# Performance work log

Measured on AMD Instinct MI355X. Metric: run time of the kernel, lower is better.

The kernel has to match this reference:

```python
import jax, jax.numpy as jnp
import numpy as np
from math import sqrt

RELATIVE_CUTOFF = 128
VALUE_DIM = 64


def _skew(m):
    # m: (b, h, S, 2S-1) -> (b, h, S, S), out[i, j] = m[i, j - i + S - 1]
    b, h, S, _ = m.shape
    m = jnp.pad(m, ((0, 0), (0, 0), (0, 0), (0, 1)))          # (b,h,S,2S)
    m = m.reshape(b, h, 2 * S * S)
    m = jnp.pad(m, ((0, 0), (0, 0), (0, S - 1)))
    m = m.reshape(b, h, S + 1, 2 * S - 1)
    return m[:, :, :S, S - 1:]


def setup_inputs() -> dict:
    key = jax.random.key(0)
    ks = jax.random.split(key, 5)
    B, S, E, H, Dk, Dv = 2, 2048, 512, 8, 64, 64
    return {
        "xs": jax.random.normal(ks[0], (B, S, E), dtype=jnp.float32),
        "w_q": jax.random.normal(ks[1], (H, E, Dk), dtype=jnp.float32) * (1.0 / sqrt(E)),
        "w_k": jax.random.normal(ks[2], (H, E, Dk), dtype=jnp.float32) * (1.0 / sqrt(E)),
        "w_v": jax.random.normal(ks[3], (H, E, Dv), dtype=jnp.float32) * (1.0 / sqrt(E)),
        "w_o": jnp.ones((H,), dtype=jnp.float32),
        "a_k": jax.random.normal(ks[4], (2 * RELATIVE_CUTOFF + 1, Dk), dtype=jnp.float32) * 0.1,
    }


def reference(xs, w_q, w_k, w_v, w_o, a_k):
    S = xs.shape[1]
    queries = jnp.einsum("bse,heq->bhsq", xs, w_q)
    keys = jnp.einsum("bse,hek->bhsk", xs, w_k)
    values = jnp.einsum("bse,hev->bhsv", xs, w_v)

    # relative positional embeddings: pos in [-S+1, S-1], clamped to cutoff
    pos = jnp.clip(jnp.arange(-S + 1, S), -RELATIVE_CUTOFF, RELATIVE_CUTOFF) + RELATIVE_CUTOFF
    rel = a_k[pos]                                             # (2S-1, Dk)

    q_k = jnp.einsum("bhiq,bhjq->bhij", queries, keys)
    q_rel = _skew(jnp.einsum("bhiq,rq->bhir", queries, rel))   # (b,h,S,S)

    e = (q_k + q_rel) / sqrt(VALUE_DIM)
    alphas = jax.nn.softmax(e, axis=3)
    z = jnp.einsum("bhij,bhjv->bhiv", alphas, values)
    return jnp.einsum("bhsv,h->bsv", z, w_o)
```

## Files before the change

kernel.cpp:

```cpp
#include <hip/hip_runtime.h>
#include <hip/hip_bf16.h>

#define S_LEN 2048
#define E_DIM 512
#define D_DIM 64
#define H_NUM 8
#define B_NUM 2
#define BH_NUM 16
#define NQA 257
#define QAE_W 512
#define KSPLIT 2
#define KV_PER (S_LEN / KSPLIT)
#define NT (KV_PER / 64)
#define QTILE 256

typedef _Float16 half8 __attribute__((ext_vector_type(8)));
typedef float f32x16 __attribute__((ext_vector_type(16)));
typedef unsigned int uint2v __attribute__((ext_vector_type(2)));
typedef unsigned int uint4v __attribute__((ext_vector_type(4)));

static __device__ __forceinline__ f32x16 MFMA(half8 a, half8 b, f32x16 c) {
    return __builtin_amdgcn_mfma_f32_32x32x16_f16(a, b, c, 0, 0, 0);
}
static __device__ __forceinline__ f32x16 ZERO16() {
    f32x16 z;
    #pragma unroll
    for (int i = 0; i < 16; ++i) z[i] = 0.f;
    return z;
}
static __device__ __forceinline__ unsigned int PKRTZ(float a, float b) {
    return __builtin_bit_cast(unsigned int, __builtin_amdgcn_cvt_pkrtz(a, b));
}

__global__ __launch_bounds__(256) void cast_x_kernel(
    const float* __restrict__ xs, _Float16* __restrict__ Xh)
{
    const int idx = (blockIdx.x * 256 + threadIdx.x) * 8;
    float4 a = *(const float4*)&xs[idx];
    float4 b = *(const float4*)&xs[idx + 4];
    half8 o;
    o[0] = (_Float16)a.x; o[1] = (_Float16)a.y; o[2] = (_Float16)a.z; o[3] = (_Float16)a.w;
    o[4] = (_Float16)b.x; o[5] = (_Float16)b.y; o[6] = (_Float16)b.z; o[7] = (_Float16)b.w;
    *(half8*)&Xh[idx] = o;
}

__global__ __launch_bounds__(256) void cast_wak_kernel(
    const float* __restrict__ w_q, const float* __restrict__ w_k,
    const float* __restrict__ w_v, const float* __restrict__ w_o,
    const float* __restrict__ a_k,
    _Float16* __restrict__ Wht, _Float16* __restrict__ akh)
{
    __shared__ float T[64][68];
    const int type = blockIdx.z;
    const int t = threadIdx.x;
    if (type == 3) {
        const int bn = blockIdx.y * 8 + blockIdx.x;
        if (bn >= 9) return;
        const int idx = (bn * 256 + t) * 8;
        if (idx < NQA * 64) {
            float4 a = *(const float4*)&a_k[idx];
            float4 b = *(const float4*)&a_k[idx + 4];
            half8 o;
            o[0] = (_Float16)a.x; o[1] = (_Float16)a.y; o[2] = (_Float16)a.z; o[3] = (_Float16)a.w;
            o[4] = (_Float16)b.x; o[5] = (_Float16)b.y; o[6] = (_Float16)b.z; o[7] = (_Float16)b.w;
            *(half8*)&akh[idx] = o;
        }
        return;
    }
    const int kt = blockIdx.x, h = blockIdx.y;
    const float* W = (type == 0) ? w_q : (type == 1) ? w_k : w_v;
    const float scale = (type == 0) ? 0.125f : (type == 2 ? w_o[h] : 1.0f);
    const int kr = t >> 2, nseg = (t & 3) * 16;
    #pragma unroll
    for (int i = 0; i < 4; ++i)
        *(float4*)&T[kr][nseg + 4 * i] =
            *(const float4*)&W[((size_t)h * 512 + kt * 64 + kr) * 64 + nseg + 4 * i];
    __syncthreads();
    const int nr = t >> 2, kseg = (t & 3) * 16;
    _Float16* dst = Wht + ((size_t)(type * 8 + h) * 64 + nr) * 512 + kt * 64 + kseg;
    #pragma unroll
    for (int i = 0; i < 2; ++i) {
        half8 o;
        #pragma unroll
        for (int j = 0; j < 8; ++j) o[j] = (_Float16)(T[kseg + 8 * i + j][nr] * scale);
        *(half8*)&dst[8 * i] = o;
    }
}

__global__ __launch_bounds__(256) void proj_mfma_kernel(
    const _Float16* __restrict__ Xh, const _Float16* __restrict__ Wht,
    _Float16* __restrict__ Qh, _Float16* __restrict__ Kh,
    _Float16* __restrict__ Vt)
{
    __shared__ _Float16 Xlds[2][128][72];
    __shared__ _Float16 Wlds[2][64][72];

    const int mt = blockIdx.x, bh = blockIdx.y, type = blockIdx.z;
    const int b = bh >> 3, h = bh & 7;
    const int m0 = mt * 128;
    const int t = threadIdx.x, wid = t >> 6, lane = t & 63;
    const int lq = lane & 31, lh = lane >> 5;

    const _Float16* W = Wht + (size_t)(type * 8 + h) * 64 * 512;
    const _Float16* X = Xh + ((size_t)b * S_LEN + m0) * 512;

    const int xrow = t >> 1, xseg = (t & 1) * 32;
    const int wrow = t >> 2, wseg = (t & 3) * 16;

    #pragma unroll
    for (int i = 0; i < 4; ++i)
        *(half8*)&Xlds[0][xrow][xseg + 8 * i] =
            *(const half8*)&X[(size_t)xrow * 512 + xseg + 8 * i];
    #pragma unroll
    for (int i = 0; i < 2; ++i)
        *(half8*)&Wlds[0][wrow][wseg + 8 * i] =
            *(const half8*)&W[(size_t)wrow * 512 + wseg + 8 * i];
    __syncthreads();

    f32x16 acc[2];
    acc[0] = ZERO16(); acc[1] = ZERO16();
    int cur = 0;
    for (int c = 0; c < 8; ++c) {
        half8 xst[4], wst[2];
        if (c < 7) {
            const int k0 = (c + 1) * 64;
            #pragma unroll
            for (int i = 0; i < 4; ++i)
                xst[i] = *(const half8*)&X[(size_t)xrow * 512 + k0 + xseg + 8 * i];
            #pragma unroll
            for (int i = 0; i < 2; ++i)
                wst[i] = *(const half8*)&W[(size_t)wrow * 512 + k0 + wseg + 8 * i];
        }
        #pragma unroll
        for (int kc = 0; kc < 4; ++kc) {
            half8 a  = *(const half8*)&Xlds[cur][wid * 32 + lq][kc * 16 + lh * 8];
            half8 b0 = *(const half8*)&Wlds[cur][lq][kc * 16 + lh * 8];
            half8 b1 = *(const half8*)&Wlds[cur][32 + lq][kc * 16 + lh * 8];
            acc[0] = MFMA(a, b0, acc[0]);
            acc[1] = MFMA(a, b1, acc[1]);
        }
        if (c < 7) {
            #pragma unroll
            for (int i = 0; i < 4; ++i)
                *(half8*)&Xlds[cur ^ 1][xrow][xseg + 8 * i] = xst[i];
            #pragma unroll
            for (int i = 0; i < 2; ++i)
                *(half8*)&Wlds[cur ^ 1][wrow][wseg + 8 * i] = wst[i];
        }
        __syncthreads();
        cur ^= 1;
    }

    _Float16* ob = &Wlds[0][0][0];
    #pragma unroll
    for (int n = 0; n < 2; ++n)
        #pragma unroll
        for (int r = 0; r < 16; ++r) {
            int row = wid * 32 + (r & 3) + ((r >> 2) << 3) + (lh << 2);
            ob[row * 72 + n * 32 + lq] = (_Float16)acc[n][r];
        }
    __syncthreads();

    if (type == 2) {
        const int v = t >> 2, sseg = (t & 3) * 32;
        _Float16* dst = Vt + ((size_t)bh * 64 + v) * S_LEN + m0 + sseg;
        #pragma unroll
        for (int i = 0; i < 4; ++i) {
            half8 o;
            #pragma unroll
            for (int j = 0; j < 8; ++j) o[j] = ob[(sseg + 8 * i + j) * 72 + v];
            *(half8*)&dst[8 * i] = o;
        }
    } else {
        _Float16* P = (type == 0) ? Qh : Kh;
        const int row = t >> 1, seg = (t & 1) * 32;
        _Float16* dst = P + ((size_t)bh * S_LEN + m0 + row) * 64 + seg;
        #pragma unroll
        for (int i = 0; i < 4; ++i)
            *(half8*)&dst[8 * i] = *(const half8*)&ob[row * 72 + seg + 8 * i];
    }
}

__global__ __launch_bounds__(256) void qa_mfma_kernel(
    const _Float16* __restrict__ Qh, const _Float16* __restrict__ akh,
    _Float16* __restrict__ QAe)
{
    __shared__ _Float16 ak[288][72];
    __shared__ _Float16 SLo[128], SHi[128];
    const int m0 = blockIdx.x * 128, bh = blockIdx.y;
    const int t = threadIdx.x, wid = t >> 6, lane = t & 63;
    const int lq = lane & 31, lh = lane >> 5;

    for (int r = t; r < 288; r += 256) {
        if (r < NQA) {
            #pragma unroll
            for (int i = 0; i < 8; ++i)
                *(half8*)&ak[r][8 * i] = *(const half8*)&akh[(size_t)r * 64 + 8 * i];
        } else {
            half8 z = {};
            #pragma unroll
            for (int i = 0; i < 8; ++i) *(half8*)&ak[r][8 * i] = z;
        }
    }
    __syncthreads();

    const int qg = m0 + wid * 32 + lq;
    half8 qfr[4];
    #pragma unroll
    for (int kc = 0; kc < 4; ++kc)
        qfr[kc] = *(const half8*)&Qh[((size_t)bh * S_LEN + qg) * 64 + kc * 16 + lh * 8];

    for (int nsub = 0; nsub < 9; ++nsub) {
        f32x16 acc = ZERO16();
        #pragma unroll
        for (int kc = 0; kc < 4; ++kc) {
            half8 bf = *(const half8*)&ak[nsub * 32 + lq][kc * 16 + lh * 8];
            acc = MFMA(qfr[kc], bf, acc);
        }
        const int col = nsub * 32 + lq;
        if (col < NQA) {
            #pragma unroll
            for (int r = 0; r < 16; ++r) {
                const int row = m0 + wid * 32 + (r & 3) + ((r >> 2) << 3) + (lh << 2);
                const _Float16 v = (_Float16)acc[r];
                QAe[((size_t)bh * S_LEN + row) * QAE_W + col + 128] = v;
                if (col == 0)   SLo[row - m0] = v;
                if (col == 256) SHi[row - m0] = v;
            }
        }
    }
    __syncthreads();

    const int prow = t >> 1, pseg = (t & 1) * 64;
    const _Float16 lo = SLo[prow], hi = SHi[prow];
    half8 vlo, vhi;
    #pragma unroll
    for (int j = 0; j < 8; ++j) { vlo[j] = lo; vhi[j] = hi; }
    _Float16* pb = QAe + ((size_t)bh * S_LEN + m0 + prow) * QAE_W;
    #pragma unroll
    for (int i = 0; i < 8; ++i) {
        *(half8*)&pb[pseg + 8 * i] = vlo;
        *(half8*)&pb[384 + pseg + 8 * i] = vhi;
    }
}

__global__ __launch_bounds__(512) void attn_kernel(
    const _Float16* __restrict__ Qh, const _Float16* __restrict__ Kh,
    const _Float16* __restrict__ Vt, const _Float16* __restrict__ QAe,
    _Float16* __restrict__ Po, float2* __restrict__ Ml)
{
    __shared__ __align__(16) char smraw[36864];
    _Float16 (*Klds)[64][72] = (_Float16(*)[64][72])smraw;
    _Float16 (*Vlds)[64][72] = (_Float16(*)[64][72])(smraw + 18432);
    _Float16* Obuf = (_Float16*)smraw;
    __shared__ __align__(16) _Float16 Bnd[8][32][128];

    const int p0 = blockIdx.x;
    const int nb = (p0 & 7) * 32 + (p0 >> 3);
    const int bh = nb >> 4;
    const int rem = nb & 15;
    const int qt = rem & 7, ks = rem >> 3;
    const int i0 = qt * QTILE, k0 = ks * KV_PER;

    const int t = threadIdx.x, wid = t >> 6, lane = t & 63;
    const int lq = lane & 31, lh = lane >> 5;
    const int i0w = i0 + wid * 32;
    const int qg = i0w + lq;

    int mode = 0;
    if (k0 >= i0 + QTILE - 1 + 128) mode = 1;
    else if (k0 + KV_PER - 1 <= i0 - 128) mode = 2;

    half8 qf[4];
    #pragma unroll
    for (int kc = 0; kc < 4; ++kc)
        qf[kc] = *(const half8*)&Qh[((size_t)bh * S_LEN + qg) * 64 + kc * 16 + lh * 8];

    const _Float16* qaeRow = QAe + ((size_t)bh * S_LEN + qg) * QAE_W;
    const float qa_lo = (float)qaeRow[128];
    const float qa_hi = (float)qaeRow[384];
    const _Float16* BndSrc = QAe + ((size_t)bh * S_LEN + i0w) * QAE_W;

    float rm = -1e30f, rl = 0.f;
    f32x16 acco[2];
    acco[0] = ZERO16(); acco[1] = ZERO16();

    const int srow = t >> 3, sseg = (t & 7) * 8;
    const _Float16* Kbase = Kh + ((size_t)bh * S_LEN + k0) * 64;
    const _Float16* Vbase = Vt + ((size_t)bh * 64 + srow) * S_LEN + k0;

    const int brow = lane >> 4;
    const int bcol = (lane & 15) * 8;

    half8 kst, vst, breg[8];
    *(half8*)&Klds[0][srow][sseg] = *(const half8*)&Kbase[(size_t)srow * 64 + sseg];
    *(half8*)&Vlds[0][srow][sseg] = *(const half8*)&Vbase[sseg];
    kst = *(const half8*)&Kbase[(size_t)(64 + srow) * 64 + sseg];
    vst = *(const half8*)&Vbase[64 + sseg];

    bool inb_next;
    {
        const int d0 = k0 - i0w;
        inb_next = (mode == 0) && (d0 < 159) && (d0 > -191);
        if (inb_next) {
            const int cw0n = (d0 + 225) & ~7;
            #pragma unroll
            for (int ps = 0; ps < 8; ++ps)
                breg[ps] = *(const half8*)&BndSrc[(size_t)(ps * 4 + brow) * QAE_W + cw0n + bcol];
        }
    }
    __syncthreads();

    for (int jt = 0; jt < NT; ++jt) {
        const int cur = jt & 1;
        if (jt) __syncthreads();
        if (jt + 1 < NT) {
            *(half8*)&Klds[cur ^ 1][srow][sseg] = kst;
            *(half8*)&Vlds[cur ^ 1][srow][sseg] = vst;
        }
        if (jt + 2 < NT) {
            const int jg = (jt + 2) * 64;
            kst = *(const half8*)&Kbase[(size_t)(jg + srow) * 64 + sseg];
            vst = *(const half8*)&Vbase[jg + sseg];
        }

        const int diff = k0 + jt * 64 - i0w;
        const bool inband = inb_next;
        const int cw0 = (diff + 225) & ~7;

        if (inband) {
            #pragma unroll
            for (int ps = 0; ps < 8; ++ps)
                *(half8*)&Bnd[wid][ps * 4 + brow][bcol] = breg[ps];
        }
        {
            const int dn = diff + 64;
            inb_next = (jt + 1 < NT) && (mode == 0) && (dn < 159) && (dn > -191);
            if (inb_next) {
                const int cw0n = (dn + 225) & ~7;
                #pragma unroll
                for (int ps = 0; ps < 8; ++ps)
                    breg[ps] = *(const half8*)&BndSrc[(size_t)(ps * 4 + brow) * QAE_W + cw0n + bcol];
            }
        }

        f32x16 accs[2];
        accs[0] = ZERO16(); accs[1] = ZERO16();
        __builtin_amdgcn_s_setprio(1);
        #pragma unroll
        for (int kc = 0; kc < 4; ++kc) {
            half8 ka = *(const half8*)&Klds[cur][lq][kc * 16 + lh * 8];
            half8 kb = *(const half8*)&Klds[cur][32 + lq][kc * 16 + lh * 8];
            accs[0] = MFMA(ka, qf[kc], accs[0]);
            accs[1] = MFMA(kb, qf[kc], accs[1]);
        }
        __builtin_amdgcn_s_setprio(0);

        const bool allhi = (mode == 1) || (mode == 0 && diff >= 159);
        const bool alllo = (mode == 2) || (mode == 0 && diff <= -191);
        float bunif = 0.f;
        if (allhi) bunif = qa_hi;
        else if (alllo) bunif = qa_lo;
        else {
            asm volatile("s_waitcnt lgkmcnt(0)" ::: "memory");
            __builtin_amdgcn_sched_barrier(0);
            const int pb = diff + 256 - cw0 - lq;
            #pragma unroll
            for (int m = 0; m < 2; ++m)
                #pragma unroll
                for (int r = 0; r < 16; ++r) {
                    const int keyoff = m * 32 + (r & 3) + ((r >> 2) << 3) + (lh << 2);
                    accs[m][r] += (float)Bnd[wid][lq][pb + keyoff];
                }
        }

        float t8[8];
        #pragma unroll
        for (int i = 0; i < 8; ++i)
            t8[i] = fmaxf(fmaxf(accs[0][i], accs[0][i + 8]),
                          fmaxf(accs[1][i], accs[1][i + 8]));
        float tmax = fmaxf(fmaxf(fmaxf(t8[0], t8[1]), fmaxf(t8[2], t8[3])),
                           fmaxf(fmaxf(t8[4], t8[5]), fmaxf(t8[6], t8[7])));
        tmax = fmaxf(tmax, __shfl_xor(tmax, 32));
        const float mnew = fmaxf(rm, tmax + bunif);
        const bool resc = __any(mnew > rm);
        const float corr = __expf(rm - mnew);
        const float shift = mnew - bunif;
        rm = mnew;

        #pragma unroll
        for (int m = 0; m < 2; ++m)
            #pragma unroll
            for (int r = 0; r < 16; ++r)
                accs[m][r] = __expf(accs[m][r] - shift);

        float s8[8];
        #pragma unroll
        for (int i = 0; i < 8; ++i)
            s8[i] = (accs[0][i] + accs[0][i + 8]) + (accs[1][i] + accs[1][i + 8]);
        float psum = ((s8[0] + s8[1]) + (s8[2] + s8[3])) +
                     ((s8[4] + s8[5]) + (s8[6] + s8[7]));
        psum += __shfl_xor(psum, 32);

        if (resc) {
            rl = rl * corr + psum;
            #pragma unroll
            for (int n = 0; n < 2; ++n)
                #pragma unroll
                for (int r = 0; r < 16; ++r) acco[n][r] *= corr;
        } else {
            rl += psum;
        }

        half8 pf[4];
        #pragma unroll
        for (int kc = 0; kc < 4; ++kc) {
            const int m = kc >> 1, rb = (kc & 1) * 8;
            unsigned int a01 = PKRTZ(accs[m][rb + 0], accs[m][rb + 1]);
            unsigned int a45 = PKRTZ(accs[m][rb + 4], accs[m][rb + 5]);
            unsigned int a23 = PKRTZ(accs[m][rb + 2], accs[m][rb + 3]);
            unsigned int a67 = PKRTZ(accs[m][rb + 6], accs[m][rb + 7]);
            uint2v r02 = __builtin_amdgcn_permlane32_swap(a01, a45, false, false);
            uint2v r13 = __builtin_amdgcn_permlane32_swap(a23, a67, false, false);
            uint4v wv;
            wv[0] = r02[0]; wv[1] = r13[0]; wv[2] = r02[1]; wv[3] = r13[1];
            pf[kc] = __builtin_bit_cast(half8, wv);
        }

        __builtin_amdgcn_s_setprio(1);
        #pragma unroll
        for (int kc = 0; kc < 4; ++kc) {
            half8 v0 = *(const half8*)&Vlds[cur][lq][kc * 16 + lh * 8];
            half8 v1 = *(const half8*)&Vlds[cur][32 + lq][kc * 16 + lh * 8];
            acco[0] = MFMA(v0, pf[kc], acco[0]);
            acco[1] = MFMA(v1, pf[kc], acco[1]);
        }
        __builtin_amdgcn_s_setprio(0);
    }

    __syncthreads();
    const int orow = wid * 32 + lq;
    #pragma unroll
    for (int n = 0; n < 2; ++n)
        #pragma unroll
        for (int rq = 0; rq < 4; ++rq) {
            uint2v hv;
            hv[0] = PKRTZ(acco[n][rq * 4 + 0], acco[n][rq * 4 + 1]);
            hv[1] = PKRTZ(acco[n][rq * 4 + 2], acco[n][rq * 4 + 3]);
            *(uint2v*)&Obuf[(size_t)orow * 72 + n * 32 + rq * 8 + lh * 4] = hv;
        }
    if (lh == 0)
        Ml[((size_t)ks * BH_NUM + bh) * S_LEN + qg] = make_float2(rm, rl);
    asm volatile("s_waitcnt lgkmcnt(0)" ::: "memory");
    __builtin_amdgcn_sched_barrier(0);
    const int rrow = wid * 32 + (lane >> 1);
    const int rseg = (lane & 1) * 32;
    _Float16* dst = Po + (((size_t)ks * BH_NUM + bh) * S_LEN + i0 + rrow) * 64 + rseg;
    #pragma unroll
    for (int i = 0; i < 4; ++i)
        *(half8*)&dst[8 * i] = *(const half8*)&Obuf[(size_t)rrow * 72 + rseg + 8 * i];
}

__global__ __launch_bounds__(256) void merge_kernel(
    const _Float16* __restrict__ Po, const float2* __restrict__ Ml,
    float* __restrict__ out)
{
    const int b = blockIdx.y;
    const int s = blockIdx.x * 32 + (threadIdx.x >> 3);
    const int v0 = (threadIdx.x & 7) * 8;
    float acc[8] = {0, 0, 0, 0, 0, 0, 0, 0};
    #pragma unroll
    for (int h = 0; h < 8; ++h) {
        const int bh = b * 8 + h;
        float m[KSPLIT], l[KSPLIT];
        #pragma unroll
        for (int p = 0; p < KSPLIT; ++p) {
            const float2 v = Ml[((size_t)p * BH_NUM + bh) * S_LEN + s];
            m[p] = v.x; l[p] = v.y;
        }
        float M = fmaxf(m[0], m[1]);
        float L = 0.f, w[KSPLIT];
        #pragma unroll
        for (int p = 0; p < KSPLIT; ++p) { w[p] = __expf(m[p] - M); L += w[p] * l[p]; }
        const float invL = 1.0f / L;
        #pragma unroll
        for (int p = 0; p < KSPLIT; ++p) {
            half8 o = *(const half8*)&Po[(((size_t)p * BH_NUM + bh) * S_LEN + s) * 64 + v0];
            const float wp = w[p] * invL;
            #pragma unroll
            for (int j = 0; j < 8; ++j) acc[j] += wp * (float)o[j];
        }
    }
    float4 o0 = {acc[0], acc[1], acc[2], acc[3]};
    float4 o1 = {acc[4], acc[5], acc[6], acc[7]};
    *(float4*)&out[((size_t)b * S_LEN + s) * 64 + v0] = o0;
    *(float4*)&out[((size_t)b * S_LEN + s) * 64 + v0 + 4] = o1;
}

extern "C" void kernel_launch(void* const* d_in, const int* in_sizes, int n_in,
                              void* d_out, int out_size, void* d_ws, size_t ws_size,
                              hipStream_t stream)
{
    const float* xs  = (const float*)d_in[0];
    const float* w_q = (const float*)d_in[1];
    const float* w_k = (const float*)d_in[2];
    const float* w_v = (const float*)d_in[3];
    const float* w_o = (const float*)d_in[4];
    const float* a_k = (const float*)d_in[5];
    float* out = (float*)d_out;

    char* w = (char*)d_ws;
    _Float16* Xh  = (_Float16*)w;  w += (size_t)B_NUM * S_LEN * E_DIM * 2;
    _Float16* Wht = (_Float16*)w;  w += (size_t)3 * H_NUM * 64 * 512 * 2;
    _Float16* akh = (_Float16*)w;  w += 33024;
    _Float16* Qh  = (_Float16*)w;  w += (size_t)BH_NUM * S_LEN * 64 * 2;
    _Float16* Kh  = (_Float16*)w;  w += (size_t)BH_NUM * S_LEN * 64 * 2;
    _Float16* Vt  = (_Float16*)w;  w += (size_t)BH_NUM * S_LEN * 64 * 2;
    _Float16* QAe = (_Float16*)w;  w += (size_t)BH_NUM * S_LEN * QAE_W * 2;
    _Float16* Po  = (_Float16*)w;  w += (size_t)KSPLIT * BH_NUM * S_LEN * 64 * 2;
    float2*   Ml  = (float2*)w;

    cast_x_kernel<<<1024, 256, 0, stream>>>(xs, Xh);
    cast_wak_kernel<<<dim3(8, 8, 4), 256, 0, stream>>>(w_q, w_k, w_v, w_o, a_k, Wht, akh);
    proj_mfma_kernel<<<dim3(16, 16, 3), 256, 0, stream>>>(Xh, Wht, Qh, Kh, Vt);
    qa_mfma_kernel<<<dim3(16, 16), 256, 0, stream>>>(Qh, akh, QAe);
    attn_kernel<<<256, 512, 0, stream>>>(Qh, Kh, Vt, QAe, Po, Ml);
    merge_kernel<<<dim3(64, 2), 256, 0, stream>>>(Po, Ml, out);
}
```

Baseline: 92.61 us.

## Split KV four ways with single-buffered LDS and narrower band tile

Doubles the KV split so the attention kernel launches 512 blocks instead of 256, and extends the merge kernel to combine four partial softmax results. K/V LDS tiles become single-buffered and the relative-band tile narrows to 112 columns. Together these cut shared memory per block so that launch bounds of 4 blocks per CU can fit. This targets low occupancy and underfilled CUs. The cost is an extra barrier per iteration, more partial outputs to write and merge, and loss of double-buffered overlap.

Result: slower. 138.7 us (+49.7%).

```diff
diff --git a/kernel.cpp b/kernel.cpp
--- a/kernel.cpp
+++ b/kernel.cpp
@@ -9,10 +9,11 @@
 #define BH_NUM 16
 #define NQA 257
 #define QAE_W 512
-#define KSPLIT 2
+#define KSPLIT 4
 #define KV_PER (S_LEN / KSPLIT)
 #define NT (KV_PER / 64)
 #define QTILE 256
+#define BNDW 112
 
 typedef _Float16 half8 __attribute__((ext_vector_type(8)));
 typedef float f32x16 __attribute__((ext_vector_type(16)));
@@ -244,21 +245,20 @@
     }
 }
 
-__global__ __launch_bounds__(512) void attn_kernel(
+__global__ __launch_bounds__(512, 4) void attn_kernel(
     const _Float16* __restrict__ Qh, const _Float16* __restrict__ Kh,
     const _Float16* __restrict__ Vt, const _Float16* __restrict__ QAe,
     _Float16* __restrict__ Po, float2* __restrict__ Ml)
 {
-    __shared__ __align__(16) char smraw[36864];
-    _Float16 (*Klds)[64][72] = (_Float16(*)[64][72])smraw;
-    _Float16 (*Vlds)[64][72] = (_Float16(*)[64][72])(smraw + 18432);
-    _Float16* Obuf = (_Float16*)smraw;
-    __shared__ __align__(16) _Float16 Bnd[8][32][128];
+    __shared__ __align__(16) _Float16 Klds[64][72];
+    __shared__ __align__(16) _Float16 Vlds[64][72];
+    __shared__ __align__(16) _Float16 Bnd[8][32][BNDW];
+    _Float16* Obuf = &Bnd[0][0][0];
 
     const int p0 = blockIdx.x;
-    const int nb = (p0 & 7) * 32 + (p0 >> 3);
-    const int bh = nb >> 4;
-    const int rem = nb & 15;
+    const int nb = (p0 & 7) * 64 + (p0 >> 3);
+    const int bh = nb >> 5;
+    const int rem = nb & 31;
     const int qt = rem & 7, ks = rem >> 3;
     const int i0 = qt * QTILE, k0 = ks * KV_PER;
 
@@ -289,14 +289,14 @@
     const _Float16* Kbase = Kh + ((size_t)bh * S_LEN + k0) * 64;
     const _Float16* Vbase = Vt + ((size_t)bh * 64 + srow) * S_LEN + k0;
 
-    const int brow = lane >> 4;
-    const int bcol = (lane & 15) * 8;
-
-    half8 kst, vst, breg[8];
-    *(half8*)&Klds[0][srow][sseg] = *(const half8*)&Kbase[(size_t)srow * 64 + sseg];
-    *(half8*)&Vlds[0][srow][sseg] = *(const half8*)&Vbase[sseg];
-    kst = *(const half8*)&Kbase[(size_t)(64 + srow) * 64 + sseg];
-    vst = *(const half8*)&Vbase[64 + sseg];
+    const int brow = lane >> 1;
+    const int bhalf = (lane & 1) * 56;
+
+    half8 kA, vA, kB, vB, breg[7];
+    kA = *(const half8*)&Kbase[(size_t)srow * 64 + sseg];
+    vA = *(const half8*)&Vbase[sseg];
+    kB = *(const half8*)&Kbase[(size_t)(64 + srow) * 64 + sseg];
+    vB = *(const half8*)&Vbase[64 + sseg];
 
     bool inb_next;
     {
@@ -305,23 +305,21 @@
         if (inb_next) {
             const int cw0n = (d0 + 225) & ~7;
             #pragma unroll
-            for (int ps = 0; ps < 8; ++ps)
-                breg[ps] = *(const half8*)&BndSrc[(size_t)(ps * 4 + brow) * QAE_W + cw0n + bcol];
-        }
-    }
-    __syncthreads();
-
+            for (int i = 0; i < 7; ++i)
+                breg[i] = *(const half8*)&BndSrc[(size_t)brow * QAE_W + cw0n + bhalf + i * 8];
+        }
+    }
+
+    #pragma unroll
     for (int jt = 0; jt < NT; ++jt) {
-        const int cur = jt & 1;
         if (jt) __syncthreads();
-        if (jt + 1 < NT) {
-            *(half8*)&Klds[cur ^ 1][srow][sseg] = kst;
-            *(half8*)&Vlds[cur ^ 1][srow][sseg] = vst;
-        }
+        *(half8*)&Klds[srow][sseg] = kA;
+        *(half8*)&Vlds[srow][sseg] = vA;
+        kA = kB; vA = vB;
         if (jt + 2 < NT) {
             const int jg = (jt + 2) * 64;
-            kst = *(const half8*)&Kbase[(size_t)(jg + srow) * 64 + sseg];
-            vst = *(const half8*)&Vbase[jg + sseg];
+            kB = *(const half8*)&Kbase[(size_t)(jg + srow) * 64 + sseg];
+            vB = *(const half8*)&Vbase[jg + sseg];
         }
 
         const int diff = k0 + jt * 64 - i0w;
@@ -330,8 +328,8 @@
 
         if (inband) {
             #pragma unroll
-            for (int ps = 0; ps < 8; ++ps)
-                *(half8*)&Bnd[wid][ps * 4 + brow][bcol] = breg[ps];
+            for (int i = 0; i < 7; ++i)
+                *(half8*)&Bnd[wid][brow][bhalf + i * 8] = breg[i];
         }
         {
             const int dn = diff + 64;
@@ -339,18 +337,19 @@
             if (inb_next) {
                 const int cw0n = (dn + 225) & ~7;
                 #pragma unroll
-                for (int ps = 0; ps < 8; ++ps)
-                    breg[ps] = *(const half8*)&BndSrc[(size_t)(ps * 4 + brow) * QAE_W + cw0n + bcol];
+                for (int i = 0; i < 7; ++i)
+                    breg[i] = *(const half8*)&BndSrc[(size_t)brow * QAE_W + cw0n + bhalf + i * 8];
             }
         }
+        __syncthreads();
 
         f32x16 accs[2];
         accs[0] = ZERO16(); accs[1] = ZERO16();
         __builtin_amdgcn_s_setprio(1);
         #pragma unroll
         for (int kc = 0; kc < 4; ++kc) {
-            half8 ka = *(const half8*)&Klds[cur][lq][kc * 16 + lh * 8];
-            half8 kb = *(const half8*)&Klds[cur][32 + lq][kc * 16 + lh * 8];
+            half8 ka = *(const half8*)&Klds[lq][kc * 16 + lh * 8];
+            half8 kb = *(const half8*)&Klds[32 + lq][kc * 16 + lh * 8];
             accs[0] = MFMA(ka, qf[kc], accs[0]);
             accs[1] = MFMA(kb, qf[kc], accs[1]);
         }
@@ -430,8 +429,8 @@
         __builtin_amdgcn_s_setprio(1);
         #pragma unroll
         for (int kc = 0; kc < 4; ++kc) {
-            half8 v0 = *(const half8*)&Vlds[cur][lq][kc * 16 + lh * 8];
-            half8 v1 = *(const half8*)&Vlds[cur][32 + lq][kc * 16 + lh * 8];
+            half8 v0 = *(const half8*)&Vlds[lq][kc * 16 + lh * 8];
+            half8 v1 = *(const half8*)&Vlds[32 + lq][kc * 16 + lh * 8];
             acco[0] = MFMA(v0, pf[kc], acco[0]);
             acco[1] = MFMA(v1, pf[kc], acco[1]);
         }
@@ -478,7 +477,7 @@
             const float2 v = Ml[((size_t)p * BH_NUM + bh) * S_LEN + s];
             m[p] = v.x; l[p] = v.y;
         }
-        float M = fmaxf(m[0], m[1]);
+        float M = fmaxf(fmaxf(m[0], m[1]), fmaxf(m[2], m[3]));
         float L = 0.f, w[KSPLIT];
         #pragma unroll
         for (int p = 0; p < KSPLIT; ++p) { w[p] = __expf(m[p] - M); L += w[p] * l[p]; }
@@ -524,6 +523,6 @@
     cast_wak_kernel<<<dim3(8, 8, 4), 256, 0, stream>>>(w_q, w_k, w_v, w_o, a_k, Wht, akh);
     proj_mfma_kernel<<<dim3(16, 16, 3), 256, 0, stream>>>(Xh, Wht, Qh, Kh, Vt);
     qa_mfma_kernel<<<dim3(16, 16), 256, 0, stream>>>(Qh, akh, QAe);
-    attn_kernel<<<256, 512, 0, stream>>>(Qh, Kh, Vt, QAe, Po, Ml);
+    attn_kernel<<<512, 512, 0, stream>>>(Qh, Kh, Vt, QAe, Po, Ml);
     merge_kernel<<<dim3(64, 2), 256, 0, stream>>>(Po, Ml, out);
 }
```

## Fuse query-relative projection into projection kernel and use base-2 softmax

Applied to the files above, without the earlier changes.

Folds the q·a_k relative-logit computation into the Q projection blocks, reusing the Q tile already in LDS instead of launching a separate kernel that re-reads Q from global memory. Q is pre-scaled by log2(e)/8 so the softmax can use exp2f instead of __expf in the attention and merge kernels. Shared memory is repurposed through a raw buffer with aliased views. The Q-type blocks now carry extra work, which may leave the projection grid load-imbalanced.

Result: faster. 89.94 us (-2.9%).

```diff
diff --git a/kernel.cpp b/kernel.cpp
--- a/kernel.cpp
+++ b/kernel.cpp
@@ -69,7 +69,8 @@
     }
     const int kt = blockIdx.x, h = blockIdx.y;
     const float* W = (type == 0) ? w_q : (type == 1) ? w_k : w_v;
-    const float scale = (type == 0) ? 0.125f : (type == 2 ? w_o[h] : 1.0f);
+    const float scale = (type == 0) ? 0.18033688011112042f
+                                    : (type == 2 ? w_o[h] : 1.0f);
     const int kr = t >> 2, nseg = (t & 3) * 16;
     #pragma unroll
     for (int i = 0; i < 4; ++i)
@@ -89,11 +90,17 @@
 
 __global__ __launch_bounds__(256) void proj_mfma_kernel(
     const _Float16* __restrict__ Xh, const _Float16* __restrict__ Wht,
+    const _Float16* __restrict__ akh,
     _Float16* __restrict__ Qh, _Float16* __restrict__ Kh,
-    _Float16* __restrict__ Vt)
+    _Float16* __restrict__ Vt, _Float16* __restrict__ QAe)
 {
-    __shared__ _Float16 Xlds[2][128][72];
-    __shared__ _Float16 Wlds[2][64][72];
+    __shared__ __align__(16) _Float16 raw[30208];
+    _Float16 (*Xlds)[128][72] = (_Float16(*)[128][72])raw;
+    _Float16 (*Wlds)[64][72]  = (_Float16(*)[64][72])(raw + 18432);
+    _Float16* ob  = raw;
+    _Float16 (*ak)[72] = (_Float16(*)[72])(raw + 9216);
+    _Float16* SLo = raw + 29952;
+    _Float16* SHi = raw + 30080;
 
     const int mt = blockIdx.x, bh = blockIdx.y, type = blockIdx.z;
     const int b = bh >> 3, h = bh & 7;
@@ -151,7 +158,6 @@
         cur ^= 1;
     }
 
-    _Float16* ob = &Wlds[0][0][0];
     #pragma unroll
     for (int n = 0; n < 2; ++n)
         #pragma unroll
@@ -171,7 +177,10 @@
             for (int j = 0; j < 8; ++j) o[j] = ob[(sseg + 8 * i + j) * 72 + v];
             *(half8*)&dst[8 * i] = o;
         }
-    } else {
+        return;
+    }
+
+    {
         _Float16* P = (type == 0) ? Qh : Kh;
         const int row = t >> 1, seg = (t & 1) * 32;
         _Float16* dst = P + ((size_t)bh * S_LEN + m0 + row) * 64 + seg;
@@ -179,17 +188,7 @@
         for (int i = 0; i < 4; ++i)
             *(half8*)&dst[8 * i] = *(const half8*)&ob[row * 72 + seg + 8 * i];
     }
-}
-
-__global__ __launch_bounds__(256) void qa_mfma_kernel(
-    const _Float16* __restrict__ Qh, const _Float16* __restrict__ akh,
-    _Float16* __restrict__ QAe)
-{
-    __shared__ _Float16 ak[288][72];
-    __shared__ _Float16 SLo[128], SHi[128];
-    const int m0 = blockIdx.x * 128, bh = blockIdx.y;
-    const int t = threadIdx.x, wid = t >> 6, lane = t & 63;
-    const int lq = lane & 31, lh = lane >> 5;
+    if (type != 0) return;
 
     for (int r = t; r < 288; r += 256) {
         if (r < NQA) {
@@ -204,25 +203,24 @@
     }
     __syncthreads();
 
-    const int qg = m0 + wid * 32 + lq;
     half8 qfr[4];
     #pragma unroll
     for (int kc = 0; kc < 4; ++kc)
-        qfr[kc] = *(const half8*)&Qh[((size_t)bh * S_LEN + qg) * 64 + kc * 16 + lh * 8];
+        qfr[kc] = *(const half8*)&ob[(wid * 32 + lq) * 72 + kc * 16 + lh * 8];
 
     for (int nsub = 0; nsub < 9; ++nsub) {
-        f32x16 acc = ZERO16();
+        f32x16 qa = ZERO16();
         #pragma unroll
         for (int kc = 0; kc < 4; ++kc) {
             half8 bf = *(const half8*)&ak[nsub * 32 + lq][kc * 16 + lh * 8];
-            acc = MFMA(qfr[kc], bf, acc);
+            qa = MFMA(qfr[kc], bf, qa);
         }
         const int col = nsub * 32 + lq;
         if (col < NQA) {
             #pragma unroll
             for (int r = 0; r < 16; ++r) {
                 const int row = m0 + wid * 32 + (r & 3) + ((r >> 2) << 3) + (lh << 2);
-                const _Float16 v = (_Float16)acc[r];
+                const _Float16 v = (_Float16)qa[r];
                 QAe[((size_t)bh * S_LEN + row) * QAE_W + col + 128] = v;
                 if (col == 0)   SLo[row - m0] = v;
                 if (col == 256) SHi[row - m0] = v;
@@ -384,7 +382,7 @@
         tmax = fmaxf(tmax, __shfl_xor(tmax, 32));
         const float mnew = fmaxf(rm, tmax + bunif);
         const bool resc = __any(mnew > rm);
-        const float corr = __expf(rm - mnew);
+        const float corr = exp2f(rm - mnew);
         const float shift = mnew - bunif;
         rm = mnew;
 
@@ -392,7 +390,7 @@
         for (int m = 0; m < 2; ++m)
             #pragma unroll
             for (int r = 0; r < 16; ++r)
-                accs[m][r] = __expf(accs[m][r] - shift);
+                accs[m][r] = exp2f(accs[m][r] - shift);
 
         float s8[8];
         #pragma unroll
@@ -481,7 +479,7 @@
         float M = fmaxf(m[0], m[1]);
         float L = 0.f, w[KSPLIT];
         #pragma unroll
-        for (int p = 0; p < KSPLIT; ++p) { w[p] = __expf(m[p] - M); L += w[p] * l[p]; }
+        for (int p = 0; p < KSPLIT; ++p) { w[p] = exp2f(m[p] - M); L += w[p] * l[p]; }
         const float invL = 1.0f / L;
         #pragma unroll
         for (int p = 0; p < KSPLIT; ++p) {
@@ -522,8 +520,7 @@
 
     cast_x_kernel<<<1024, 256, 0, stream>>>(xs, Xh);
     cast_wak_kernel<<<dim3(8, 8, 4), 256, 0, stream>>>(w_q, w_k, w_v, w_o, a_k, Wht, akh);
-    proj_mfma_kernel<<<dim3(16, 16, 3), 256, 0, stream>>>(Xh, Wht, Qh, Kh, Vt);
-    qa_mfma_kernel<<<dim3(16, 16), 256, 0, stream>>>(Qh, akh, QAe);
+    proj_mfma_kernel<<<dim3(16, 16, 3), 256, 0, stream>>>(Xh, Wht, akh, Qh, Kh, Vt, QAe);
     attn_kernel<<<256, 512, 0, stream>>>(Qh, Kh, Vt, QAe, Po, Ml);
     merge_kernel<<<dim3(64, 2), 256, 0, stream>>>(Po, Ml, out);
 }
```
